# Kernel tuning notes

Hardware: AMD Instinct MI355X
Metric: run time of the kernel (lower is better)

Reference implementation:

```python
import jax, jax.numpy as jnp
import numpy as np

N_HEADS = 16

def setup_inputs() -> dict:
    key = jax.random.key(0)
    k1, k2, k3 = jax.random.split(key, 3)
    B, T, C = 2, 2048, 1024
    x = jax.random.normal(k1, (B, T, C), dtype=jnp.float32)
    W_qkv = jax.random.normal(k2, (3 * C, C), dtype=jnp.float32) * 0.02
    b_qkv = jnp.zeros((3 * C,), dtype=jnp.float32)
    W_proj = jax.random.normal(k3, (C, C), dtype=jnp.float32) * 0.02
    b_proj = jnp.zeros((C,), dtype=jnp.float32)
    return {"x": x, "W_qkv": W_qkv, "b_qkv": b_qkv, "W_proj": W_proj, "b_proj": b_proj}

def reference(x, W_qkv, b_qkv, W_proj, b_proj):
    B, T, C = x.shape
    H = N_HEADS
    hd = C // H
    # fused QKV projection: (B,T,3C)
    qkv = x @ W_qkv.T + b_qkv
    # mirror torch: reshape to (B,T,H,3*hd) then chunk along last dim
    qkv = qkv.reshape(B, T, H, 3 * hd)
    q, k, v = jnp.split(qkv, 3, axis=-1)  # each (B,T,H,hd)
    q = q / jnp.sqrt(jnp.asarray(hd, dtype=q.dtype))
    # scaled dot-product attention, non-causal, full matrix (faithful to source)
    att = jnp.einsum('bihd,bjhd->bhij', q, k)  # (B,H,T,T)
    att = jax.nn.softmax(att, axis=-1)
    out = jnp.einsum('bhij,bjhd->bihd', att, v)  # (B,T,H,hd)
    out = out.reshape(B, T, C)
    return out @ W_proj.T + b_proj
```

## Files before the change

kernel.cpp:

```cpp
#include <hip/hip_runtime.h>


typedef __bf16 bf16x4 __attribute__((ext_vector_type(4)));
typedef __bf16 bf16x8 __attribute__((ext_vector_type(8)));
typedef float  f32x4  __attribute__((ext_vector_type(4)));

#define AS1(p) ((const __attribute__((address_space(1))) void*)(p))
#define AS3(p) ((__attribute__((address_space(3))) void*)(p))

__global__ __launch_bounds__(256)
void cvt_all(const float* __restrict__ a, const float* __restrict__ b,
             const float* __restrict__ c, __bf16* __restrict__ oa,
             __bf16* __restrict__ ob, __bf16* __restrict__ oc,
             int na, int nb, int nc)
{
    const int total = (na + nb + nc) >> 2;
    const int stride = gridDim.x * blockDim.x;
    for (int i4 = blockIdx.x * blockDim.x + threadIdx.x; i4 < total; i4 += stride) {
        int i = i4 << 2;
        const float* src; __bf16* dst;
        if (i < na)               { src = a + i;             dst = oa + i; }
        else if (i < na + nb)     { src = b + (i - na);      dst = ob + (i - na); }
        else                      { src = c + (i - na - nb); dst = oc + (i - na - nb); }
        const float4 v = *(const float4*)src;
        bf16x4 o = { (__bf16)v.x, (__bf16)v.y, (__bf16)v.z, (__bf16)v.w };
        *(bf16x4*)dst = o;
    }
}

template<int MODE>
__global__ __launch_bounds__(256)
void gemm_bt(const __bf16* __restrict__ A, const __bf16* __restrict__ W,
             const float* __restrict__ bias, int M, int N, int K,
             __bf16* __restrict__ O0, __bf16* __restrict__ O1,
             __bf16* __restrict__ O2, float* __restrict__ Of)
{
    __shared__ __bf16 sA[128 * 64];
    __shared__ __bf16 sB[128 * 64];
    const int tid  = threadIdx.x;
    const int w    = tid >> 6, lane = tid & 63;
    const int g    = lane >> 4, r16 = lane & 15;
    const int lin  = blockIdx.y * gridDim.x + blockIdx.x;
    const int per  = (gridDim.x * gridDim.y) >> 3;
    const int nlin = (lin & 7) * per + (lin >> 3);
    const int tM   = (nlin / gridDim.x) * 128, tN = (nlin % gridDim.x) * 128;
    const int wr   = w >> 1, wc = w & 1;
    const int crow = lane >> 3;
    const int ccol = (lane & 7) * 8;

    f32x4 acc[4][4] = {};

    for (int k0 = 0; k0 < K; k0 += 64) {
#pragma unroll
        for (int c = w; c < 16; c += 4) {
            const __bf16* ga = A + (size_t)(tM + c * 8 + crow) * K + k0 + ccol;
            __builtin_amdgcn_global_load_lds(AS1(ga), AS3(&sA[c * 8 * 64]), 16, 0, 0);
            const __bf16* gb = W + (size_t)(tN + c * 8 + crow) * K + k0 + ccol;
            __builtin_amdgcn_global_load_lds(AS1(gb), AS3(&sB[c * 8 * 64]), 16, 0, 0);
        }
        __syncthreads();
#pragma unroll
        for (int kk = 0; kk < 2; ++kk) {
            bf16x8 a[4], b[4];
#pragma unroll
            for (int mf = 0; mf < 4; ++mf)
                a[mf] = *(const bf16x8*)&sA[(wr * 64 + mf * 16 + r16) * 64 + kk * 32 + g * 8];
#pragma unroll
            for (int nf = 0; nf < 4; ++nf)
                b[nf] = *(const bf16x8*)&sB[(wc * 64 + nf * 16 + r16) * 64 + kk * 32 + g * 8];
#pragma unroll
            for (int mf = 0; mf < 4; ++mf)
#pragma unroll
                for (int nf = 0; nf < 4; ++nf)
                    acc[mf][nf] = __builtin_amdgcn_mfma_f32_16x16x32_bf16(
                        a[mf], b[nf], acc[mf][nf], 0, 0, 0);
        }
        __syncthreads();
    }

#pragma unroll
    for (int mf = 0; mf < 4; ++mf) {
#pragma unroll
        for (int nf = 0; nf < 4; ++nf) {
#pragma unroll
            for (int reg = 0; reg < 4; ++reg) {
                const int row = tM + wr * 64 + mf * 16 + g * 4 + reg;
                const int col = tN + wc * 64 + nf * 16 + r16;
                float v = acc[mf][nf][reg] + bias[col];
                if (MODE == 0) {
                    const int h = col / 192, j = col % 192;
                    const int b = row >> 11, t = row & 2047;
                    const size_t bh = (size_t)(b * 16 + h);
                    if (j < 64)
                        O0[(bh * 2048 + t) * 64 + j] = (__bf16)(v * 0.18033688011112042f);
                    else if (j < 128)
                        O1[(bh * 2048 + t) * 64 + (j - 64)] = (__bf16)v;
                    else
                        O2[(bh * 64 + (j - 128)) * 2048 + t] = (__bf16)v;
                } else {
                    Of[(size_t)row * N + col] = v;
                }
            }
        }
    }
}

__global__ __launch_bounds__(256, 4)
void attn(const __bf16* __restrict__ Q, const __bf16* __restrict__ K,
          const __bf16* __restrict__ V, __bf16* __restrict__ O)
{
    __shared__ __bf16 sK[2][64 * 64];
    __shared__ __bf16 sV[2][64 * 64];

    const int tid = threadIdx.x;
    const int w   = tid >> 6, lane = tid & 63;
    const int g   = lane >> 4, r16 = lane & 15;
    const int m   = blockIdx.x + (blockIdx.y << 5) + (blockIdx.z << 9);
    const int bh  = (m & 7) + ((m >> 8) << 3);
    const int qb  = (m >> 3) & 31;
    const int q0  = qb * 64 + w * 16;
    const __bf16* Qp = Q + (size_t)bh * 2048 * 64;
    const __bf16* Kp = K + (size_t)bh * 2048 * 64;
    const __bf16* Vp = V + (size_t)bh * 64 * 2048;

    const int srow  = lane >> 3;
    const int scolV = 8 * ((lane & 7) ^ srow);
    const int scolK = 8 * ((lane & 7) ^ ((srow & 3) | ((w & 1) << 2)));
    const int swzK  = ((r16 & 3) | (((r16 >> 2) & 1) << 2)) << 4;
    const int swzV  = (r16 & 7) << 4;

    bf16x8 qa[2];
#pragma unroll
    for (int kk = 0; kk < 2; ++kk)
        qa[kk] = *(const bf16x8*)(Qp + (size_t)(q0 + r16) * 64 + kk * 32 + g * 8);

    f32x4 o[4] = {};
    float mrun = -1e30f, lrun = 0.f;

#pragma unroll
    for (int r = 0; r < 2; ++r) {
        const int ldsb = r * 4096 + w * 1024;
        const int row  = r * 32 + w * 8 + srow;
        __builtin_amdgcn_global_load_lds(AS1(Kp + (size_t)row * 64 + scolK),
                                         AS3((char*)&sK[0][0] + ldsb), 16, 0, 0);
        __builtin_amdgcn_global_load_lds(AS1(Vp + (size_t)row * 2048 + scolV),
                                         AS3((char*)&sV[0][0] + ldsb), 16, 0, 0);
    }
    __syncthreads();

    for (int t = 0; t < 32; ++t) {
        const int cur = t & 1;
        if (t < 31) {
            const int kvn = (t + 1) * 64;
#pragma unroll
            for (int r = 0; r < 2; ++r) {
                const int ldsb = r * 4096 + w * 1024;
                const int row  = r * 32 + w * 8 + srow;
                __builtin_amdgcn_global_load_lds(AS1(Kp + (size_t)(kvn + row) * 64 + scolK),
                                                 AS3((char*)&sK[cur ^ 1][0] + ldsb), 16, 0, 0);
                __builtin_amdgcn_global_load_lds(AS1(Vp + (size_t)row * 2048 + kvn + scolV),
                                                 AS3((char*)&sV[cur ^ 1][0] + ldsb), 16, 0, 0);
            }
        }
        bf16x8 kb[4][2];
#pragma unroll
        for (int nf = 0; nf < 4; ++nf) {
            const int row = ((nf >> 1) << 5) + ((r16 >> 2) << 3) + ((nf & 1) << 2) + (r16 & 3);
#pragma unroll
            for (int kk = 0; kk < 2; ++kk)
                kb[nf][kk] = *(const bf16x8*)((const char*)&sK[cur][0] + row * 128
                                              + ((kk * 64 + g * 16) ^ swzK));
        }
        f32x4 S[4];
        __builtin_amdgcn_s_setprio(1);
#pragma unroll
        for (int nf = 0; nf < 4; ++nf) {
            f32x4 s = {};
            s = __builtin_amdgcn_mfma_f32_16x16x32_bf16(kb[nf][0], qa[0], s, 0, 0, 0);
            s = __builtin_amdgcn_mfma_f32_16x16x32_bf16(kb[nf][1], qa[1], s, 0, 0, 0);
            S[nf] = s;
        }
        __builtin_amdgcn_s_setprio(0);
        float rm = fmaxf(fmaxf(S[0][0], S[0][1]), fmaxf(S[0][2], S[0][3]));
#pragma unroll
        for (int nf = 1; nf < 4; ++nf)
            rm = fmaxf(rm, fmaxf(fmaxf(S[nf][0], S[nf][1]), fmaxf(S[nf][2], S[nf][3])));
        rm = fmaxf(rm, __shfl_xor(rm, 16));
        rm = fmaxf(rm, __shfl_xor(rm, 32));
        if (!__all(rm <= mrun + 8.f)) {
            const float mn = fmaxf(mrun, rm);
            const float al = exp2f(mrun - mn);
#pragma unroll
            for (int df = 0; df < 4; ++df)
#pragma unroll
                for (int reg = 0; reg < 4; ++reg) o[df][reg] *= al;
            lrun *= al;
            mrun = mn;
        }
        float ps = 0.f;
#pragma unroll
        for (int nf = 0; nf < 4; ++nf)
#pragma unroll
            for (int reg = 0; reg < 4; ++reg) {
                const float p = exp2f(S[nf][reg] - mrun);
                S[nf][reg] = p;
                ps += p;
            }
        lrun += ps;
        bf16x8 pb[2];
#pragma unroll
        for (int kk = 0; kk < 2; ++kk) {
            bf16x8 tpk;
            tpk[0] = (__bf16)S[kk * 2][0];     tpk[1] = (__bf16)S[kk * 2][1];
            tpk[2] = (__bf16)S[kk * 2][2];     tpk[3] = (__bf16)S[kk * 2][3];
            tpk[4] = (__bf16)S[kk * 2 + 1][0]; tpk[5] = (__bf16)S[kk * 2 + 1][1];
            tpk[6] = (__bf16)S[kk * 2 + 1][2]; tpk[7] = (__bf16)S[kk * 2 + 1][3];
            pb[kk] = tpk;
        }
        __builtin_amdgcn_s_setprio(1);
#pragma unroll
        for (int kk = 0; kk < 2; ++kk)
#pragma unroll
            for (int df = 0; df < 4; ++df) {
                const int row = df * 16 + r16;
                bf16x8 vb = *(const bf16x8*)((const char*)&sV[cur][0] + row * 128
                                             + ((kk * 64 + g * 16) ^ swzV));
                o[df] = __builtin_amdgcn_mfma_f32_16x16x32_bf16(vb, pb[kk], o[df], 0, 0, 0);
            }
        __builtin_amdgcn_s_setprio(0);
        __syncthreads();
    }

    lrun += __shfl_xor(lrun, 16);
    lrun += __shfl_xor(lrun, 32);
    const float inv = 1.f / lrun;
    const size_t token = (size_t)(bh >> 4) * 2048 + q0 + r16;
#pragma unroll
    for (int df = 0; df < 4; ++df) {
        bf16x4 ov = { (__bf16)(o[df][0] * inv), (__bf16)(o[df][1] * inv),
                      (__bf16)(o[df][2] * inv), (__bf16)(o[df][3] * inv) };
        *(bf16x4*)(O + token * 1024 + (bh & 15) * 64 + df * 16 + g * 4) = ov;
    }
}

extern "C" void kernel_launch(void* const* d_in, const int* in_sizes, int n_in,
                              void* d_out, int out_size, void* d_ws, size_t ws_size,
                              hipStream_t stream)
{
    const float* x     = (const float*)d_in[0];
    const float* Wqkv  = (const float*)d_in[1];
    const float* bqkv  = (const float*)d_in[2];
    const float* Wproj = (const float*)d_in[3];
    const float* bproj = (const float*)d_in[4];
    float* out = (float*)d_out;

    const size_t NX   = (size_t)4096 * 1024;
    const size_t NWQ  = (size_t)3072 * 1024;
    const size_t NWP  = (size_t)1024 * 1024;

    __bf16* xb  = (__bf16*)d_ws;
    __bf16* Wqb = xb  + NX;
    __bf16* Wpb = Wqb + NWQ;
    __bf16* Qs  = Wpb + NWP;
    __bf16* Ks  = Qs  + NX;
    __bf16* Vt  = Ks  + NX;
    __bf16* Os  = Vt  + NX;

    cvt_all<<<dim3(2048), dim3(256), 0, stream>>>(x, Wqkv, Wproj, xb, Wqb, Wpb,
                                                  (int)NX, (int)NWQ, (int)NWP);
    gemm_bt<0><<<dim3(24, 32), dim3(256), 0, stream>>>(xb, Wqb, bqkv, 4096, 3072, 1024, Qs, Ks, Vt, nullptr);
    attn<<<dim3(32, 16, 2), dim3(256), 0, stream>>>(Qs, Ks, Vt, Os);
    gemm_bt<1><<<dim3(8, 32), dim3(256), 0, stream>>>(Os, Wpb, bproj, 4096, 1024, 1024, nullptr, nullptr, nullptr, out);
}
```

Baseline: 144.0 us.

## Fold max subtraction into MFMA init and compute row sums with MFMA

Seeds the QK^T MFMA accumulator with -mrun so scores arrive already shifted, defers the cross-lane max shuffles to the rare rescale path, and computes the softmax denominator with an extra MFMA against a ones vector instead of scalar adds and final shuffles. The aim is fewer VALU subtracts, adds and cross-lane shuffles per KV tile in the softmax inner loop. In exchange it adds two MFMAs per tile and sums bf16-rounded probabilities, which slightly changes the numerics of the normalizer.

```diff
diff --git a/kernel.cpp b/kernel.cpp
--- a/kernel.cpp
+++ b/kernel.cpp
@@ -134,8 +134,13 @@
     for (int kk = 0; kk < 2; ++kk)
         qa[kk] = *(const bf16x8*)(Qp + (size_t)(q0 + r16) * 64 + kk * 32 + g * 8);
 
+    bf16x8 ones;
+#pragma unroll
+    for (int i = 0; i < 8; ++i) ones[i] = (__bf16)1.0f;
+
     f32x4 o[4] = {};
-    float mrun = -1e30f, lrun = 0.f;
+    f32x4 lsum = {};
+    float mrun = 0.f;
 
 #pragma unroll
     for (int r = 0; r < 2; ++r) {
@@ -171,53 +176,49 @@
                 kb[nf][kk] = *(const bf16x8*)((const char*)&sK[cur][0] + row * 128
                                               + ((kk * 64 + g * 16) ^ swzK));
         }
+        const f32x4 cinit = { -mrun, -mrun, -mrun, -mrun };
         f32x4 S[4];
         __builtin_amdgcn_s_setprio(1);
 #pragma unroll
         for (int nf = 0; nf < 4; ++nf) {
-            f32x4 s = {};
-            s = __builtin_amdgcn_mfma_f32_16x16x32_bf16(kb[nf][0], qa[0], s, 0, 0, 0);
-            s = __builtin_amdgcn_mfma_f32_16x16x32_bf16(kb[nf][1], qa[1], s, 0, 0, 0);
-            S[nf] = s;
+            f32x4 s = __builtin_amdgcn_mfma_f32_16x16x32_bf16(kb[nf][0], qa[0], cinit, 0, 0, 0);
+            S[nf]   = __builtin_amdgcn_mfma_f32_16x16x32_bf16(kb[nf][1], qa[1], s, 0, 0, 0);
         }
         __builtin_amdgcn_s_setprio(0);
         float rm = fmaxf(fmaxf(S[0][0], S[0][1]), fmaxf(S[0][2], S[0][3]));
 #pragma unroll
         for (int nf = 1; nf < 4; ++nf)
             rm = fmaxf(rm, fmaxf(fmaxf(S[nf][0], S[nf][1]), fmaxf(S[nf][2], S[nf][3])));
-        rm = fmaxf(rm, __shfl_xor(rm, 16));
-        rm = fmaxf(rm, __shfl_xor(rm, 32));
-        if (!__all(rm <= mrun + 8.f)) {
-            const float mn = fmaxf(mrun, rm);
-            const float al = exp2f(mrun - mn);
+        if (!__all(rm <= 8.f)) {
+            rm = fmaxf(rm, __shfl_xor(rm, 16));
+            rm = fmaxf(rm, __shfl_xor(rm, 32));
+            const float delta = fmaxf(rm, 0.f);
+            const float al = exp2f(-delta);
 #pragma unroll
             for (int df = 0; df < 4; ++df)
 #pragma unroll
                 for (int reg = 0; reg < 4; ++reg) o[df][reg] *= al;
-            lrun *= al;
-            mrun = mn;
-        }
-        float ps = 0.f;
-#pragma unroll
-        for (int nf = 0; nf < 4; ++nf)
-#pragma unroll
-            for (int reg = 0; reg < 4; ++reg) {
-                const float p = exp2f(S[nf][reg] - mrun);
-                S[nf][reg] = p;
-                ps += p;
-            }
-        lrun += ps;
+#pragma unroll
+            for (int reg = 0; reg < 4; ++reg) lsum[reg] *= al;
+            mrun += delta;
+#pragma unroll
+            for (int nf = 0; nf < 4; ++nf)
+#pragma unroll
+                for (int reg = 0; reg < 4; ++reg) S[nf][reg] -= delta;
+        }
         bf16x8 pb[2];
 #pragma unroll
         for (int kk = 0; kk < 2; ++kk) {
             bf16x8 tpk;
-            tpk[0] = (__bf16)S[kk * 2][0];     tpk[1] = (__bf16)S[kk * 2][1];
-            tpk[2] = (__bf16)S[kk * 2][2];     tpk[3] = (__bf16)S[kk * 2][3];
-            tpk[4] = (__bf16)S[kk * 2 + 1][0]; tpk[5] = (__bf16)S[kk * 2 + 1][1];
-            tpk[6] = (__bf16)S[kk * 2 + 1][2]; tpk[7] = (__bf16)S[kk * 2 + 1][3];
+            tpk[0] = (__bf16)exp2f(S[kk * 2][0]);     tpk[1] = (__bf16)exp2f(S[kk * 2][1]);
+            tpk[2] = (__bf16)exp2f(S[kk * 2][2]);     tpk[3] = (__bf16)exp2f(S[kk * 2][3]);
+            tpk[4] = (__bf16)exp2f(S[kk * 2 + 1][0]); tpk[5] = (__bf16)exp2f(S[kk * 2 + 1][1]);
+            tpk[6] = (__bf16)exp2f(S[kk * 2 + 1][2]); tpk[7] = (__bf16)exp2f(S[kk * 2 + 1][3]);
             pb[kk] = tpk;
         }
         __builtin_amdgcn_s_setprio(1);
+        lsum = __builtin_amdgcn_mfma_f32_16x16x32_bf16(ones, pb[0], lsum, 0, 0, 0);
+        lsum = __builtin_amdgcn_mfma_f32_16x16x32_bf16(ones, pb[1], lsum, 0, 0, 0);
 #pragma unroll
         for (int kk = 0; kk < 2; ++kk)
 #pragma unroll
@@ -231,9 +232,7 @@
         __syncthreads();
     }
 
-    lrun += __shfl_xor(lrun, 16);
-    lrun += __shfl_xor(lrun, 32);
-    const float inv = 1.f / lrun;
+    const float inv = 1.f / lsum[0];
     const size_t token = (size_t)(bh >> 4) * 2048 + q0 + r16;
 #pragma unroll
     for (int df = 0; df < 4; ++df) {
```

Measured after the change: 138.4 us. 1.04x faster.
